# Kernel optimization log

Measured on AMD Instinct MI355X. Metric: run time of the kernel, lower is better.

## Reference

```python
import jax, jax.numpy as jnp
import numpy as np

B, N, H = 4, 256, 512
P = 128  # game_physics_params


def _init(key, shape, scale=0.02):
    return jax.random.normal(key, shape, dtype=jnp.float32) * scale


def setup_inputs() -> dict:
    key = jax.random.key(0)
    ks = jax.random.split(key, 16)
    return {
        "object_features": jax.random.normal(ks[0], (B, N, H), dtype=jnp.float32),
        # physics_predictor: H -> 512 -> P
        "pp_w1": _init(ks[1], (H, 512)), "pp_b1": jnp.zeros((512,), jnp.float32),
        "pp_w2": _init(ks[2], (512, P)), "pp_b2": jnp.zeros((P,), jnp.float32),
        # collision_detector: 2H -> 256 -> 128 -> 1
        "cd_w1": _init(ks[3], (2 * H, 256)), "cd_b1": jnp.zeros((256,), jnp.float32),
        "cd_w2": _init(ks[4], (256, 128)), "cd_b2": jnp.zeros((128,), jnp.float32),
        "cd_w3": _init(ks[5], (128, 1)), "cd_b3": jnp.zeros((1,), jnp.float32),
        # velocity / force heads: H -> 3
        "vel_w": _init(ks[6], (H, 3)), "vel_b": jnp.zeros((3,), jnp.float32),
        "frc_w": _init(ks[7], (H, 3)), "frc_b": jnp.zeros((3,), jnp.float32),
    }


def reference(object_features, pp_w1, pp_b1, pp_w2, pp_b2,
              cd_w1, cd_b1, cd_w2, cd_b2, cd_w3, cd_b3,
              vel_w, vel_b, frc_w, frc_b):
    x = object_features  # [B, N, H]
    # physics predictor MLP
    p = jax.nn.relu(x @ pp_w1 + pp_b1) @ pp_w2 + pp_b2  # [B, N, P]
    mass = jax.nn.sigmoid(p[..., 0:1]) * 100.0
    friction = jax.nn.sigmoid(p[..., 1:2])
    elasticity = jax.nn.sigmoid(p[..., 2:3])
    density = jax.nn.sigmoid(p[..., 3:4]) * 10.0
    velocities = x @ vel_w + vel_b  # [B, N, 3]
    forces = x @ frc_w + frc_b      # [B, N, 3]

    # vectorized pairwise collision detection over upper-triangle pairs
    iu, ju = np.triu_indices(N, k=1)  # static index arrays, length Np = N(N-1)/2
    pairs = jnp.concatenate([x[:, iu], x[:, ju]], axis=-1)  # [B, Np, 2H]
    h = jax.nn.relu(pairs @ cd_w1 + cd_b1)
    h = jax.nn.relu(h @ cd_w2 + cd_b2)
    prob = jax.nn.sigmoid(h @ cd_w3 + cd_b3)[..., 0]  # [B, Np]
    collision_matrix = jnp.zeros((x.shape[0], N, N), dtype=x.dtype)
    collision_matrix = collision_matrix.at[:, iu, ju].set(prob).at[:, ju, iu].set(prob)

    return (mass, friction, elasticity, density, velocities, forces, collision_matrix)
```

## Files before the change

### kernel.cpp

```cpp
#include <hip/hip_runtime.h>
#include <hip/hip_bf16.h>

typedef __attribute__((ext_vector_type(8))) short bf16x8;
typedef __attribute__((ext_vector_type(4))) float f32x4;

__device__ __forceinline__ float sigmoidf_(float v) {
    return 1.0f / (1.0f + __expf(-v));
}
__device__ __forceinline__ short f2bf(float f) {
    union { __hip_bfloat16 h; short s; } cv;
    cv.h = __float2bfloat16(f);
    return cv.s;
}
__device__ __forceinline__ float bf2f(short s) {
    union { float f; unsigned u; } cv;
    cv.u = ((unsigned)(unsigned short)s) << 16;
    return cv.f;
}

__global__ __launch_bounds__(256) void convert_kernel(
    const float* __restrict__ x, const float* __restrict__ pp_w1,
    const float* __restrict__ cd_w1, const float* __restrict__ cd_w2,
    const float* __restrict__ pp_w2, const float* __restrict__ vel_w,
    const float* __restrict__ frc_w,
    __hip_bfloat16* __restrict__ xb, __hip_bfloat16* __restrict__ Wt,
    __hip_bfloat16* __restrict__ w2t, float* __restrict__ hw)
{
    __shared__ float ts[64][65];
    const int b = blockIdx.x, t = threadIdx.x;

    if (b < 256) {
        int base = b * 2048 + t * 8;
        float4 a = *(const float4*)(x + base);
        float4 c = *(const float4*)(x + base + 4);
        bf16x8 o;
        o[0] = f2bf(a.x); o[1] = f2bf(a.y); o[2] = f2bf(a.z); o[3] = f2bf(a.w);
        o[4] = f2bf(c.x); o[5] = f2bf(c.y); o[6] = f2bf(c.z); o[7] = f2bf(c.w);
        *(bf16x8*)(xb + base) = o;
        return;
    }
    if (b == 392) {
        for (int e = t; e < 5120; e += 256) {
            int h = e >> 9, k = e & 511;
            float v = (h < 4) ? pp_w2[k * 128 + h]
                    : (h < 7) ? vel_w[k * 3 + (h - 4)]
                              : frc_w[k * 3 + (h - 7)];
            hw[e] = v;
        }
        return;
    }

    const float* src; int ss, k0, n0, region;
    if (b < 320)      { int i = b - 256; src = pp_w1; ss = 512; k0 = (i >> 3) * 64; n0 = (i & 7) * 64; region = 0; }
    else if (b < 384) { int i = b - 320; src = cd_w1; ss = 256; k0 = (i >> 2) * 64; n0 = (i & 3) * 64; region = 1; }
    else              { int i = b - 384; src = cd_w2; ss = 128; k0 = (i >> 1) * 64; n0 = (i & 1) * 64; region = 2; }

    #pragma unroll
    for (int i = 0; i < 4; ++i) {
        int r = (t >> 4) + i * 16, c4 = (t & 15) * 4;
        *(float4*)&ts[r][c4] = *(const float4*)(src + (k0 + r) * ss + n0 + c4);
    }
    __syncthreads();
    #pragma unroll
    for (int i = 0; i < 4; ++i) {
        int nOut = (t >> 4) + i * 16, kc = (t & 15) * 4;
        ushort4 o;
        o.x = (unsigned short)f2bf(ts[kc + 0][nOut]);
        o.y = (unsigned short)f2bf(ts[kc + 1][nOut]);
        o.z = (unsigned short)f2bf(ts[kc + 2][nOut]);
        o.w = (unsigned short)f2bf(ts[kc + 3][nOut]);
        int gn = n0 + nOut, gk = k0 + kc;
        if (region == 0)      *(ushort4*)(Wt + gn * 512 + gk) = o;
        else if (region == 1) {
            int row = (gk < 512) ? (512 + gn) : (768 + gn);
            *(ushort4*)(Wt + row * 512 + (gk & 511)) = o;
        } else                *(ushort4*)(w2t + gn * 256 + gk) = o;
    }
}

__global__ __launch_bounds__(256) void gemm_kernel(
    const __hip_bfloat16* __restrict__ xb, const __hip_bfloat16* __restrict__ Wt,
    const float* __restrict__ pp_b1, const float* __restrict__ cd_b1,
    __hip_bfloat16* __restrict__ hidg, float* __restrict__ Ug,
    float* __restrict__ Vg)
{
    const int t = threadIdx.x;
    const int wave = t >> 6, lane = t & 63;
    const int l = lane & 15, q = lane >> 4;
    const int m0 = blockIdx.y * 32;
    const int n0 = blockIdx.x * 128 + wave * 32;

    const __hip_bfloat16* a0p = xb + (m0 + l) * 512 + q * 8;
    const __hip_bfloat16* a1p = a0p + 16 * 512;
    const __hip_bfloat16* b0p = Wt + (n0 + l) * 512 + q * 8;
    const __hip_bfloat16* b1p = b0p + 16 * 512;

    f32x4 acc00 = {}, acc01 = {}, acc10 = {}, acc11 = {};
    #pragma unroll
    for (int ks = 0; ks < 16; ++ks) {
        bf16x8 a0 = *(const bf16x8*)(a0p + ks * 32);
        bf16x8 a1 = *(const bf16x8*)(a1p + ks * 32);
        bf16x8 b0 = *(const bf16x8*)(b0p + ks * 32);
        bf16x8 b1 = *(const bf16x8*)(b1p + ks * 32);
        acc00 = __builtin_amdgcn_mfma_f32_16x16x32_bf16(a0, b0, acc00, 0, 0, 0);
        acc01 = __builtin_amdgcn_mfma_f32_16x16x32_bf16(a0, b1, acc01, 0, 0, 0);
        acc10 = __builtin_amdgcn_mfma_f32_16x16x32_bf16(a1, b0, acc10, 0, 0, 0);
        acc11 = __builtin_amdgcn_mfma_f32_16x16x32_bf16(a1, b1, acc11, 0, 0, 0);
    }

    const int c0 = n0 + l, c1 = n0 + 16 + l;
    #pragma unroll
    for (int mt = 0; mt < 2; ++mt) {
        const f32x4& A0 = mt ? acc10 : acc00;
        const f32x4& A1 = mt ? acc11 : acc01;
        if (n0 < 512) {
            float b0v = pp_b1[c0], b1v = pp_b1[c1];
            #pragma unroll
            for (int r = 0; r < 4; ++r) {
                int rg = m0 + mt * 16 + q * 4 + r;
                hidg[rg * 512 + c0] = __float2bfloat16(fmaxf(A0[r] + b0v, 0.f));
                hidg[rg * 512 + c1] = __float2bfloat16(fmaxf(A1[r] + b1v, 0.f));
            }
        } else if (n0 < 768) {
            float b0v = cd_b1[c0 - 512], b1v = cd_b1[c1 - 512];
            #pragma unroll
            for (int r = 0; r < 4; ++r) {
                int rg = m0 + mt * 16 + q * 4 + r;
                Ug[rg * 256 + (c0 - 512)] = A0[r] + b0v;
                Ug[rg * 256 + (c1 - 512)] = A1[r] + b1v;
            }
        } else {
            #pragma unroll
            for (int r = 0; r < 4; ++r) {
                int rg = m0 + mt * 16 + q * 4 + r;
                Vg[rg * 256 + (c0 - 768)] = A0[r];
                Vg[rg * 256 + (c1 - 768)] = A1[r];
            }
        }
    }
}

__global__ __launch_bounds__(256) void heads_kernel(
    const float* __restrict__ x, const __hip_bfloat16* __restrict__ hidg,
    const float* __restrict__ hw, const float* __restrict__ pp_b2,
    const float* __restrict__ vel_b, const float* __restrict__ frc_b,
    float* __restrict__ out)
{
    const int t = threadIdx.x, wave = t >> 6, lane = t & 63;
    const int row = blockIdx.x * 4 + wave;

    const float4* xr = (const float4*)(x + row * 512);
    float4 xa = xr[lane * 2], xc = xr[lane * 2 + 1];
    bf16x8 hb = *(const bf16x8*)(hidg + row * 512 + lane * 8);
    float hf[8];
    #pragma unroll
    for (int j = 0; j < 8; ++j) hf[j] = bf2f(hb[j]);

    #pragma unroll
    for (int h = 0; h < 10; ++h) {
        const float4* wr = (const float4*)(hw + h * 512);
        float4 wa = wr[lane * 2], wc = wr[lane * 2 + 1];
        float s;
        if (h < 4) {
            s = hf[0]*wa.x + hf[1]*wa.y + hf[2]*wa.z + hf[3]*wa.w
              + hf[4]*wc.x + hf[5]*wc.y + hf[6]*wc.z + hf[7]*wc.w;
        } else {
            s = xa.x*wa.x + xa.y*wa.y + xa.z*wa.z + xa.w*wa.w
              + xc.x*wc.x + xc.y*wc.y + xc.z*wc.z + xc.w*wc.w;
        }
        s += __shfl_xor(s, 1);  s += __shfl_xor(s, 2);
        s += __shfl_xor(s, 4);  s += __shfl_xor(s, 8);
        s += __shfl_xor(s, 16); s += __shfl_xor(s, 32);
        if (lane == 0) {
            if (h < 4) {
                float sg = sigmoidf_(s + pp_b2[h]);
                out[h * 1024 + row] = (h == 0) ? sg * 100.f : (h == 3) ? sg * 10.f : sg;
            } else if (h < 7) {
                out[4096 + row * 3 + (h - 4)] = s + vel_b[h - 4];
            } else {
                out[7168 + row * 3 + (h - 7)] = s + frc_b[h - 7];
            }
        }
    }
}

__global__ __launch_bounds__(256) void pair_kernel(
    const float* __restrict__ Ug, const float* __restrict__ Vg,
    const __hip_bfloat16* __restrict__ w2t,
    const float* __restrict__ cd_b2, const float* __restrict__ cd_w3,
    const float* __restrict__ cd_b3, float* __restrict__ cm)
{
    const int b = blockIdx.y;
    const int tp = blockIdx.x;
    int ti = 0;
    while ((ti + 1) * (33 - (ti + 1)) / 2 <= tp) ++ti;
    const int tj = ti + (tp - ti * (33 - ti) / 2);

    __shared__ __align__(16) float Us[16][260];
    __shared__ __align__(16) float Vs[16][260];

    const int t = threadIdx.x;
    const int i0 = ti * 16, j0 = tj * 16;

    {
        const int row = t >> 4, c0 = (t & 15) * 16;
        const float* Up = Ug + (b * 256 + i0 + row) * 256 + c0;
        const float* Vp = Vg + (b * 256 + j0 + row) * 256 + c0;
        #pragma unroll
        for (int i = 0; i < 4; ++i) {
            *(float4*)&Us[row][c0 + i * 4] = *(const float4*)(Up + i * 4);
            *(float4*)&Vs[row][c0 + i * 4] = *(const float4*)(Vp + i * 4);
        }
    }
    __syncthreads();

    const int wave = t >> 6, lane = t & 63;
    const int l = lane & 15, q = lane >> 4;

    f32x4 acc[4][8] = {};
    const __hip_bfloat16* wB = w2t + l * 256 + q * 8;

    #pragma unroll
    for (int ks = 0; ks < 8; ++ks) {
        bf16x8 bfr[8];
        #pragma unroll
        for (int nt = 0; nt < 8; ++nt)
            bfr[nt] = *(const bf16x8*)(wB + nt * 16 * 256 + ks * 32);
        const int kk = ks * 32 + q * 8;
        #pragma unroll
        for (int mt = 0; mt < 4; ++mt) {
            const int mtg = wave * 4 + mt;
            float4 u0 = *(const float4*)&Us[mtg][kk];
            float4 u1 = *(const float4*)&Us[mtg][kk + 4];
            float4 v0 = *(const float4*)&Vs[l][kk];
            float4 v1 = *(const float4*)&Vs[l][kk + 4];
            bf16x8 afr;
            afr[0] = f2bf(fmaxf(u0.x + v0.x, 0.f));
            afr[1] = f2bf(fmaxf(u0.y + v0.y, 0.f));
            afr[2] = f2bf(fmaxf(u0.z + v0.z, 0.f));
            afr[3] = f2bf(fmaxf(u0.w + v0.w, 0.f));
            afr[4] = f2bf(fmaxf(u1.x + v1.x, 0.f));
            afr[5] = f2bf(fmaxf(u1.y + v1.y, 0.f));
            afr[6] = f2bf(fmaxf(u1.z + v1.z, 0.f));
            afr[7] = f2bf(fmaxf(u1.w + v1.w, 0.f));
            #pragma unroll
            for (int nt = 0; nt < 8; ++nt)
                acc[mt][nt] = __builtin_amdgcn_mfma_f32_16x16x32_bf16(
                    afr, bfr[nt], acc[mt][nt], 0, 0, 0);
        }
    }

    float b2v[8], w3v[8];
    #pragma unroll
    for (int nt = 0; nt < 8; ++nt) {
        b2v[nt] = cd_b2[nt * 16 + l];
        w3v[nt] = cd_w3[nt * 16 + l];
    }
    const float b3 = cd_b3[0];
    float* base = cm + b * 65536;
    #pragma unroll
    for (int mt = 0; mt < 4; ++mt) {
        const int i = i0 + wave * 4 + mt;
        #pragma unroll
        for (int r = 0; r < 4; ++r) {
            float s = 0.f;
            #pragma unroll
            for (int nt = 0; nt < 8; ++nt)
                s += fmaxf(acc[mt][nt][r] + b2v[nt], 0.f) * w3v[nt];
            s += __shfl_xor(s, 1);
            s += __shfl_xor(s, 2);
            s += __shfl_xor(s, 4);
            s += __shfl_xor(s, 8);
            if (l == 0) {
                const int j = j0 + q * 4 + r;
                float prob = sigmoidf_(s + b3);
                if (i < j) {
                    base[i * 256 + j] = prob;
                    base[j * 256 + i] = prob;
                } else if (i == j) {
                    base[i * 256 + i] = 0.0f;
                }
            }
        }
    }
}

extern "C" void kernel_launch(void* const* d_in, const int* in_sizes, int n_in,
                              void* d_out, int out_size, void* d_ws, size_t ws_size,
                              hipStream_t stream) {
    const float* x     = (const float*)d_in[0];
    const float* pp_w1 = (const float*)d_in[1];
    const float* pp_b1 = (const float*)d_in[2];
    const float* pp_w2 = (const float*)d_in[3];
    const float* pp_b2 = (const float*)d_in[4];
    const float* cd_w1 = (const float*)d_in[5];
    const float* cd_b1 = (const float*)d_in[6];
    const float* cd_w2 = (const float*)d_in[7];
    const float* cd_b2 = (const float*)d_in[8];
    const float* cd_w3 = (const float*)d_in[9];
    const float* cd_b3 = (const float*)d_in[10];
    const float* vel_w = (const float*)d_in[11];
    const float* vel_b = (const float*)d_in[12];
    const float* frc_w = (const float*)d_in[13];
    const float* frc_b = (const float*)d_in[14];

    float* out = (float*)d_out;
    float* Ug = (float*)d_ws;
    float* Vg = Ug + 262144;
    __hip_bfloat16* xb   = (__hip_bfloat16*)(Vg + 262144);
    __hip_bfloat16* Wt   = xb + 524288;
    __hip_bfloat16* hidg = Wt + 524288;
    __hip_bfloat16* w2t  = hidg + 524288;
    float* hw = (float*)(w2t + 32768);

    convert_kernel<<<dim3(393), dim3(256), 0, stream>>>(
        x, pp_w1, cd_w1, cd_w2, pp_w2, vel_w, frc_w, xb, Wt, w2t, hw);
    gemm_kernel<<<dim3(8, 32), dim3(256), 0, stream>>>(
        xb, Wt, pp_b1, cd_b1, hidg, Ug, Vg);
    heads_kernel<<<dim3(256), dim3(256), 0, stream>>>(
        x, hidg, hw, pp_b2, vel_b, frc_b, out);
    pair_kernel<<<dim3(136, 4), dim3(256), 0, stream>>>(
        Ug, Vg, w2t, cd_b2, cd_w3, cd_b3, out + 10240);
}
```

Baseline: 144.3 us.

## Restructure pair kernel: stage W2 in LDS, 8x8 pair tiles, two batches per block

The pair kernel now stages the full bf16 W2 (cd_w2 transposed) in shared memory once per block, so the per-wave global loads of B fragments go away. Tiles shrink from 16x16 to 8x8 object pairs, giving 528 triangular tiles, and each 512-thread block covers two batches. U/V rows are read straight from global memory, with no LDS staging, as each MFMA A fragment is built. This raises block count and parallelism, but each tile now reloads all of W2 into LDS and U/V rows are read redundantly from global/L2.

```diff
diff --git a/kernel.cpp b/kernel.cpp
--- a/kernel.cpp
+++ b/kernel.cpp
@@ -184,69 +184,65 @@
     }
 }
 
-__global__ __launch_bounds__(256) void pair_kernel(
+__global__ __launch_bounds__(512, 4) void pair_kernel(
     const float* __restrict__ Ug, const float* __restrict__ Vg,
     const __hip_bfloat16* __restrict__ w2t,
     const float* __restrict__ cd_b2, const float* __restrict__ cd_w3,
     const float* __restrict__ cd_b3, float* __restrict__ cm)
 {
-    const int b = blockIdx.y;
+    __shared__ __align__(16) short w2s[32 * 128 * 8];
+
     const int tp = blockIdx.x;
+    const int bz = blockIdx.y;
     int ti = 0;
-    while ((ti + 1) * (33 - (ti + 1)) / 2 <= tp) ++ti;
-    const int tj = ti + (tp - ti * (33 - ti) / 2);
-
-    __shared__ __align__(16) float Us[16][260];
-    __shared__ __align__(16) float Vs[16][260];
+    while ((ti + 1) * (65 - (ti + 1)) / 2 <= tp) ++ti;
+    const int tj = ti + (tp - ti * (65 - ti) / 2);
+    const int i0 = ti * 8, j0 = tj * 8;
 
     const int t = threadIdx.x;
-    const int i0 = ti * 16, j0 = tj * 16;
 
     {
-        const int row = t >> 4, c0 = (t & 15) * 16;
-        const float* Up = Ug + (b * 256 + i0 + row) * 256 + c0;
-        const float* Vp = Vg + (b * 256 + j0 + row) * 256 + c0;
         #pragma unroll
-        for (int i = 0; i < 4; ++i) {
-            *(float4*)&Us[row][c0 + i * 4] = *(const float4*)(Up + i * 4);
-            *(float4*)&Vs[row][c0 + i * 4] = *(const float4*)(Vp + i * 4);
+        for (int it = 0; it < 8; ++it) {
+            int e = it * 512 + t;
+            int n = e >> 5, g = e & 31;
+            uint4 d = *(const uint4*)(w2t + n * 256 + g * 8);
+            *(uint4*)(w2s + (g * 128 + n) * 8) = d;
         }
     }
     __syncthreads();
 
-    const int wave = t >> 6, lane = t & 63;
+    const int w = t >> 6, lane = t & 63;
+    const int qd = w & 3;
+    const int b = bz * 2 + (w >> 2);
     const int l = lane & 15, q = lane >> 4;
 
-    f32x4 acc[4][8] = {};
-    const __hip_bfloat16* wB = w2t + l * 256 + q * 8;
-
+    const int pb = qd * 16 + l;
+    const float* Up = Ug + (b * 256 + i0 + (pb >> 3)) * 256;
+    const float* Vp = Vg + (b * 256 + j0 + (pb & 7)) * 256;
+
+    f32x4 acc[8] = {};
     #pragma unroll
     for (int ks = 0; ks < 8; ++ks) {
-        bf16x8 bfr[8];
+        const int kk = ks * 32 + q * 8;
+        float4 u0 = *(const float4*)(Up + kk);
+        float4 u1 = *(const float4*)(Up + kk + 4);
+        float4 v0 = *(const float4*)(Vp + kk);
+        float4 v1 = *(const float4*)(Vp + kk + 4);
+        bf16x8 afr;
+        afr[0] = f2bf(fmaxf(u0.x + v0.x, 0.f));
+        afr[1] = f2bf(fmaxf(u0.y + v0.y, 0.f));
+        afr[2] = f2bf(fmaxf(u0.z + v0.z, 0.f));
+        afr[3] = f2bf(fmaxf(u0.w + v0.w, 0.f));
+        afr[4] = f2bf(fmaxf(u1.x + v1.x, 0.f));
+        afr[5] = f2bf(fmaxf(u1.y + v1.y, 0.f));
+        afr[6] = f2bf(fmaxf(u1.z + v1.z, 0.f));
+        afr[7] = f2bf(fmaxf(u1.w + v1.w, 0.f));
+        const short* wg = w2s + (ks * 4 + q) * 128 * 8;
         #pragma unroll
-        for (int nt = 0; nt < 8; ++nt)
-            bfr[nt] = *(const bf16x8*)(wB + nt * 16 * 256 + ks * 32);
-        const int kk = ks * 32 + q * 8;
-        #pragma unroll
-        for (int mt = 0; mt < 4; ++mt) {
-            const int mtg = wave * 4 + mt;
-            float4 u0 = *(const float4*)&Us[mtg][kk];
-            float4 u1 = *(const float4*)&Us[mtg][kk + 4];
-            float4 v0 = *(const float4*)&Vs[l][kk];
-            float4 v1 = *(const float4*)&Vs[l][kk + 4];
-            bf16x8 afr;
-            afr[0] = f2bf(fmaxf(u0.x + v0.x, 0.f));
-            afr[1] = f2bf(fmaxf(u0.y + v0.y, 0.f));
-            afr[2] = f2bf(fmaxf(u0.z + v0.z, 0.f));
-            afr[3] = f2bf(fmaxf(u0.w + v0.w, 0.f));
-            afr[4] = f2bf(fmaxf(u1.x + v1.x, 0.f));
-            afr[5] = f2bf(fmaxf(u1.y + v1.y, 0.f));
-            afr[6] = f2bf(fmaxf(u1.z + v1.z, 0.f));
-            afr[7] = f2bf(fmaxf(u1.w + v1.w, 0.f));
-            #pragma unroll
-            for (int nt = 0; nt < 8; ++nt)
-                acc[mt][nt] = __builtin_amdgcn_mfma_f32_16x16x32_bf16(
-                    afr, bfr[nt], acc[mt][nt], 0, 0, 0);
+        for (int nt = 0; nt < 8; ++nt) {
+            bf16x8 bfr = *(const bf16x8*)(wg + (nt * 16 + l) * 8);
+            acc[nt] = __builtin_amdgcn_mfma_f32_16x16x32_bf16(afr, bfr, acc[nt], 0, 0, 0);
         }
     }
 
@@ -259,27 +255,24 @@
     const float b3 = cd_b3[0];
     float* base = cm + b * 65536;
     #pragma unroll
-    for (int mt = 0; mt < 4; ++mt) {
-        const int i = i0 + wave * 4 + mt;
+    for (int r = 0; r < 4; ++r) {
+        float s = 0.f;
         #pragma unroll
-        for (int r = 0; r < 4; ++r) {
-            float s = 0.f;
-            #pragma unroll
-            for (int nt = 0; nt < 8; ++nt)
-                s += fmaxf(acc[mt][nt][r] + b2v[nt], 0.f) * w3v[nt];
-            s += __shfl_xor(s, 1);
-            s += __shfl_xor(s, 2);
-            s += __shfl_xor(s, 4);
-            s += __shfl_xor(s, 8);
-            if (l == 0) {
-                const int j = j0 + q * 4 + r;
-                float prob = sigmoidf_(s + b3);
-                if (i < j) {
-                    base[i * 256 + j] = prob;
-                    base[j * 256 + i] = prob;
-                } else if (i == j) {
-                    base[i * 256 + i] = 0.0f;
-                }
+        for (int nt = 0; nt < 8; ++nt)
+            s += fmaxf(acc[nt][r] + b2v[nt], 0.f) * w3v[nt];
+        s += __shfl_xor(s, 1);
+        s += __shfl_xor(s, 2);
+        s += __shfl_xor(s, 4);
+        s += __shfl_xor(s, 8);
+        if (l == 0) {
+            const int p = qd * 16 + q * 4 + r;
+            const int i = i0 + (p >> 3), j = j0 + (p & 7);
+            float prob = sigmoidf_(s + b3);
+            if (i < j) {
+                base[i * 256 + j] = prob;
+                base[j * 256 + i] = prob;
+            } else if (i == j) {
+                base[i * 256 + i] = 0.0f;
             }
         }
     }
@@ -319,6 +312,6 @@
         xb, Wt, pp_b1, cd_b1, hidg, Ug, Vg);
     heads_kernel<<<dim3(256), dim3(256), 0, stream>>>(
         x, hidg, hw, pp_b2, vel_b, frc_b, out);
-    pair_kernel<<<dim3(136, 4), dim3(256), 0, stream>>>(
+    pair_kernel<<<dim3(528, 2), dim3(512), 0, stream>>>(
         Ug, Vg, w2t, cd_b2, cd_w3, cd_b3, out + 10240);
 }
```

Result: faster. 140.8 us (-2.4%).
